# Kernel tuning notes

Hardware: AMD Instinct MI355X
Metric: run time of the kernel (lower is better)

Reference implementation:

```python
import jax, jax.numpy as jnp
import numpy as np

B, N, C_IN = 4, 2048, 64
HID, HEADS, NQ = 128, 4, 16
D = HID // HEADS  # per-head dim = 32
NEG_SLOPE = 0.2
MASK_VAL = -1e9


def setup_inputs() -> dict:
    key = jax.random.key(0)
    ks = jax.random.split(key, 8)
    x = jax.random.normal(ks[0], (B, N, C_IN), dtype=jnp.float32)
    adj = jax.random.randint(ks[1], (N, N), 0, 2, dtype=jnp.int32)
    # lin_in: Linear(in_channels, hidden_dim)
    W_in = jax.random.normal(ks[2], (C_IN, HID), dtype=jnp.float32) / np.sqrt(C_IN)
    b_in = jnp.zeros((HID,), dtype=jnp.float32)
    # attention vectors [1, heads, d]
    att_src = jax.random.normal(ks[3], (1, HEADS, D), dtype=jnp.float32) * 0.1
    att_dst = jax.random.normal(ks[4], (1, HEADS, D), dtype=jnp.float32) * 0.1
    # output_head: Linear(num_nodes*hidden_dim, num_qubits)
    W_out = jax.random.normal(ks[5], (N * HID, NQ), dtype=jnp.float32) / np.sqrt(N * HID)
    b_out = jnp.zeros((NQ,), dtype=jnp.float32)
    return {"x": x, "adj": adj, "W_in": W_in, "b_in": b_in,
            "att_src": att_src, "att_dst": att_dst,
            "W_out": W_out, "b_out": b_out}


def reference(x, adj, W_in, b_in, att_src, att_dst, W_out, b_out):
    b, n, _ = x.shape
    h = (x @ W_in + b_in).reshape(b, n, HEADS, D)          # [B,N,H,D]
    alpha_src = jnp.sum(h * att_src, axis=-1)               # [B,N,H]
    alpha_dst = jnp.sum(h * att_dst, axis=-1)               # [B,N,H]
    # additive scores: score[b,i,j,h] = src[b,i,h] + dst[b,j,h]
    scores = alpha_src[:, :, None, :] + alpha_dst[:, None, :, :]  # [B,N,N,H]
    scores = jnp.where(scores >= 0, scores, NEG_SLOPE * scores)   # leaky relu
    mask = (adj == 0)[None, :, :, None]                     # [1,N,N,1]
    scores = jnp.where(mask, MASK_VAL, scores)
    alpha = jax.nn.softmax(scores, axis=2)                  # softmax over neighbors j
    # dropout p=0.0 (eval) -> identity
    out = jnp.einsum('bijh,bjhd->bihd', alpha, h)           # [B,N,H,D]
    out = out.reshape(b, n * HEADS * D)                     # [B, N*HID]
    return out @ W_out + b_out                              # [B, NQ]
```

## Files before the change

kernel.cpp:

```cpp
#include <hip/hip_runtime.h>
#include <math.h>

#define BB 4
#define NN 2048
#define CIN 64
#define HID 128
#define HEADS 4
#define DD 32
#define NQ 16
#define KTOT (NN*HID)
#define LOG2E 1.44269504088896340736f
#define NEGBIG_BITS 0xC2C80000u

#define HB 512
#define AB 2048

typedef __attribute__((ext_vector_type(8))) _Float16 half8;
typedef __attribute__((ext_vector_type(4))) _Float16 half4;
typedef __attribute__((ext_vector_type(2))) _Float16 half2;
typedef __attribute__((ext_vector_type(4))) float f32x4;
typedef __attribute__((ext_vector_type(4))) unsigned uint4v;

__global__ __launch_bounds__(256) void k_pre(
    const float* __restrict__ x, const float* __restrict__ W_in,
    const float* __restrict__ b_in, const float* __restrict__ att_src,
    const float* __restrict__ att_dst, const int* __restrict__ adj,
    _Float16* __restrict__ hH, float* __restrict__ srcA, float* __restrict__ dstA,
    unsigned* __restrict__ adjb, const float* __restrict__ b_out,
    float* __restrict__ dout)
{
    __shared__ float Wl[CIN * HID];
    __shared__ float xl[16][CIN];
    const int t = threadIdx.x;

    if (blockIdx.x >= HB) {
        const int bid = blockIdx.x - HB;
        if (bid == 0 && t < 64) dout[t] = b_out[t & 15];
        const int gid = bid * 256 + t;
        const int lane = t & 63;
        const int4* p = (const int4*)(adj + (size_t)gid * 8);
        const int4 a = p[0], b = p[1];
        unsigned byte =
            (a.x != 0 ? 1u : 0u)  | (a.y != 0 ? 2u : 0u)  | (a.z != 0 ? 4u : 0u)  | (a.w != 0 ? 8u : 0u) |
            (b.x != 0 ? 16u : 0u) | (b.y != 0 ? 32u : 0u) | (b.z != 0 ? 64u : 0u) | (b.w != 0 ? 128u : 0u);
        unsigned u = byte | (((unsigned)__shfl_xor((int)byte, 1, 64)) << 8);
        u = u | (((unsigned)__shfl_xor((int)u, 2, 64)) << 16);
        if ((lane & 3) == 0) adjb[gid >> 2] = u;
        return;
    }

    const int jj0 = blockIdx.x * 16;
    {
        const float4* Ws = (const float4*)W_in;
        float4* Wd = (float4*)Wl;
#pragma unroll
        for (int u = 0; u < 8; ++u) Wd[t + 256 * u] = Ws[t + 256 * u];
        ((float4*)&xl[0][0])[t] = ((const float4*)(x + (size_t)jj0 * CIN))[t];
    }
    __syncthreads();

    const int c = t & 127, rg = t >> 7;
    const int b = jj0 >> 11, j0 = (jj0 & (NN - 1)) + rg * 8;
    const int h = c >> 5;

    float acc[8];
    const float bc = b_in[c];
#pragma unroll
    for (int rr = 0; rr < 8; ++rr) acc[rr] = bc;

#pragma unroll
    for (int k4 = 0; k4 < CIN; k4 += 4) {
        const float w0 = Wl[(k4 + 0) * HID + c];
        const float w1 = Wl[(k4 + 1) * HID + c];
        const float w2 = Wl[(k4 + 2) * HID + c];
        const float w3 = Wl[(k4 + 3) * HID + c];
#pragma unroll
        for (int rr = 0; rr < 8; ++rr) {
            const float4 xv = *(const float4*)&xl[rg * 8 + rr][k4];
            acc[rr] = fmaf(xv.w, w3, fmaf(xv.z, w2, fmaf(xv.y, w1, fmaf(xv.x, w0, acc[rr]))));
        }
    }

    half8 hv;
#pragma unroll
    for (int rr = 0; rr < 8; ++rr) hv[rr] = (_Float16)acc[rr];
    *(half8*)(hH + (size_t)(b * HID + c) * NN + j0) = hv;

    const float as = att_src[c], ad = att_dst[c];
#pragma unroll
    for (int rr = 0; rr < 8; ++rr) {
        float vs = acc[rr] * as, vd = acc[rr] * ad;
#pragma unroll
        for (int m = 16; m >= 1; m >>= 1) {
            vs += __shfl_xor(vs, m, 64);
            vd += __shfl_xor(vd, m, 64);
        }
        if ((t & 31) == 0) {
            srcA[(size_t)(b * HEADS + h) * NN + j0 + rr] = vs * LOG2E;
            dstA[(size_t)(b * HEADS + h) * NN + j0 + rr] = vd * LOG2E;
        }
    }
}

__global__ __launch_bounds__(512, 4) void k_attn(
    const unsigned* __restrict__ adjb, const _Float16* __restrict__ hH,
    const float* __restrict__ srcA, const float* __restrict__ dstA,
    _Float16* __restrict__ P, float* __restrict__ S)
{
    __shared__ float redA[8][32][36];
    __shared__ float redS[8][32];

    const int t = threadIdx.x;
    const int lane = t & 63;
    const int w = t >> 6;
    const int h = w & 3;
    const int bx = blockIdx.x;
    const int jh = bx >> 8;
    const int b = (bx >> 6) & 3;
    const int i0 = (bx & 63) * 32;
    const int jstart = jh * 1024 + (w >> 2) * 512;

    const int r16 = lane & 15;
    const int g = lane >> 4;
    const float srci0 = srcA[(size_t)(b * HEADS + h) * NN + i0 + r16];
    const float srci1 = srcA[(size_t)(b * HEADS + h) * NN + i0 + 16 + r16];
    const uint2* adjr0 = (const uint2*)(adjb + (size_t)(i0 + r16) * (NN / 32)) + (jstart >> 6);
    const uint2* adjr1 = (const uint2*)(adjb + (size_t)(i0 + 16 + r16) * (NN / 32)) + (jstart >> 6);
    const _Float16* bbase = hH + ((size_t)(b * HID) + h * DD + r16) * NN + jstart + 8 * g;
    const float4* dst4 = (const float4*)(dstA + (size_t)(b * HEADS + h) * NN + jstart) + 2 * g;

    f32x4 acc00 = {0.f, 0.f, 0.f, 0.f};
    f32x4 acc01 = {0.f, 0.f, 0.f, 0.f};
    f32x4 acc10 = {0.f, 0.f, 0.f, 0.f};
    f32x4 acc11 = {0.f, 0.f, 0.f, 0.f};
    f32x4 accS0 = {0.f, 0.f, 0.f, 0.f};
    f32x4 accS1 = {0.f, 0.f, 0.f, 0.f};
    const half8 ones = {(_Float16)1.f, (_Float16)1.f, (_Float16)1.f, (_Float16)1.f,
                        (_Float16)1.f, (_Float16)1.f, (_Float16)1.f, (_Float16)1.f};

    auto MAKEAF = [&](float srci, unsigned bits, const float* dv) -> half8 {
        float wv[8];
#pragma unroll
        for (int e = 0; e < 8; ++e) {
            float s = srci + dv[e];
            s = fmaxf(s, 0.2f * s);
            const unsigned m = (unsigned)(((int)(bits << (31 - e))) >> 31);
            const unsigned su = __builtin_bit_cast(unsigned, s);
            const unsigned sel = (su & m) | (NEGBIG_BITS & ~m);
            wv[e] = __builtin_amdgcn_exp2f(__builtin_bit_cast(float, sel));
        }
        uint4v uu;
        uu[0] = __builtin_bit_cast(unsigned, __builtin_amdgcn_cvt_pkrtz(wv[0], wv[1]));
        uu[1] = __builtin_bit_cast(unsigned, __builtin_amdgcn_cvt_pkrtz(wv[2], wv[3]));
        uu[2] = __builtin_bit_cast(unsigned, __builtin_amdgcn_cvt_pkrtz(wv[4], wv[5]));
        uu[3] = __builtin_bit_cast(unsigned, __builtin_amdgcn_cvt_pkrtz(wv[6], wv[7]));
        return __builtin_bit_cast(half8, uu);
    };

    auto GROUP = [&](unsigned w0, unsigned w1, float4 da, float4 db, half8 bb0, half8 bb1) {
        const unsigned bits0 = w0 >> (8 * g);
        const unsigned bits1 = w1 >> (8 * g);
        const float dv[8] = {da.x, da.y, da.z, da.w, db.x, db.y, db.z, db.w};
        const half8 af0 = MAKEAF(srci0, bits0, dv);
        const half8 af1 = MAKEAF(srci1, bits1, dv);
        acc00 = __builtin_amdgcn_mfma_f32_16x16x32_f16(af0, bb0, acc00, 0, 0, 0);
        acc01 = __builtin_amdgcn_mfma_f32_16x16x32_f16(af0, bb1, acc01, 0, 0, 0);
        acc10 = __builtin_amdgcn_mfma_f32_16x16x32_f16(af1, bb0, acc10, 0, 0, 0);
        acc11 = __builtin_amdgcn_mfma_f32_16x16x32_f16(af1, bb1, acc11, 0, 0, 0);
        accS0 = __builtin_amdgcn_mfma_f32_16x16x32_f16(af0, ones, accS0, 0, 0, 0);
        accS1 = __builtin_amdgcn_mfma_f32_16x16x32_f16(af1, ones, accS1, 0, 0, 0);
    };

    uint2 aA0 = adjr0[0], aA1 = adjr1[0];
    half8 bA0 = *(const half8*)(bbase);
    half8 bA1 = *(const half8*)(bbase + 32);
    half8 bA2 = *(const half8*)(bbase + 16 * NN);
    half8 bA3 = *(const half8*)(bbase + 16 * NN + 32);
    __builtin_amdgcn_sched_barrier(0);

#pragma unroll
    for (int p = 0; p < 4; ++p) {
        const int itB = 2 * p + 1;
        const uint2 aB0 = adjr0[itB], aB1 = adjr1[itB];
        const half8 bB0 = *(const half8*)(bbase + itB * 64);
        const half8 bB1 = *(const half8*)(bbase + itB * 64 + 32);
        const half8 bB2 = *(const half8*)(bbase + 16 * NN + itB * 64);
        const half8 bB3 = *(const half8*)(bbase + 16 * NN + itB * 64 + 32);
        __builtin_amdgcn_sched_barrier(0);

        {
            const int it = 2 * p;
            GROUP(aA0.x, aA1.x, dst4[it * 16],     dst4[it * 16 + 1], bA0, bA2);
            GROUP(aA0.y, aA1.y, dst4[it * 16 + 8], dst4[it * 16 + 9], bA1, bA3);
        }
        __builtin_amdgcn_sched_barrier(0);

        if (p < 3) {
            const int itA = 2 * p + 2;
            aA0 = adjr0[itA]; aA1 = adjr1[itA];
            bA0 = *(const half8*)(bbase + itA * 64);
            bA1 = *(const half8*)(bbase + itA * 64 + 32);
            bA2 = *(const half8*)(bbase + 16 * NN + itA * 64);
            bA3 = *(const half8*)(bbase + 16 * NN + itA * 64 + 32);
        }
        __builtin_amdgcn_sched_barrier(0);

        GROUP(aB0.x, aB1.x, dst4[itB * 16],     dst4[itB * 16 + 1], bB0, bB2);
        GROUP(aB0.y, aB1.y, dst4[itB * 16 + 8], dst4[itB * 16 + 9], bB1, bB3);
        __builtin_amdgcn_sched_barrier(0);
    }

#pragma unroll
    for (int r = 0; r < 4; ++r) {
        redA[w][ 0 + 4 * g + r][ 0 + r16] = acc00[r];
        redA[w][ 0 + 4 * g + r][16 + r16] = acc01[r];
        redA[w][16 + 4 * g + r][ 0 + r16] = acc10[r];
        redA[w][16 + 4 * g + r][16 + r16] = acc11[r];
    }
    if (r16 == 0) {
#pragma unroll
        for (int r = 0; r < 4; ++r) {
            redS[w][ 0 + 4 * g + r] = accS0[r];
            redS[w][16 + 4 * g + r] = accS1[r];
        }
    }
    __syncthreads();

    {
        const int i = t & 31;
        const int u = t >> 5;
        const int h2 = u & 3;
        const int d0 = (u >> 2) * 8;
        const float4 va0 = *(const float4*)&redA[h2][i][d0];
        const float4 va1 = *(const float4*)&redA[h2][i][d0 + 4];
        const float4 vb0 = *(const float4*)&redA[h2 + 4][i][d0];
        const float4 vb1 = *(const float4*)&redA[h2 + 4][i][d0 + 4];
        const float rs = redS[h2][i] + redS[h2 + 4][i];
        const half2 q0 = __builtin_bit_cast(half2, __builtin_amdgcn_cvt_pkrtz(va0.x + vb0.x, va0.y + vb0.y));
        const half2 q1 = __builtin_bit_cast(half2, __builtin_amdgcn_cvt_pkrtz(va0.z + vb0.z, va0.w + vb0.w));
        const half2 q2 = __builtin_bit_cast(half2, __builtin_amdgcn_cvt_pkrtz(va1.x + vb1.x, va1.y + vb1.y));
        const half2 q3 = __builtin_bit_cast(half2, __builtin_amdgcn_cvt_pkrtz(va1.z + vb1.z, va1.w + vb1.w));
        half8 o;
        o[0] = q0[0]; o[1] = q0[1]; o[2] = q1[0]; o[3] = q1[1];
        o[4] = q2[0]; o[5] = q2[1]; o[6] = q3[0]; o[7] = q3[1];
        *(half8*)(P + ((size_t)(jh * BB + b) * NN + i0 + i) * HID + h2 * DD + d0) = o;
        if (u < 4)
            S[((size_t)(jh * BB + b) * NN + i0 + i) * HEADS + h2] = rs;
    }
}

__global__ __launch_bounds__(256) void k_proj(
    const _Float16* __restrict__ P, const float* __restrict__ S,
    const float* __restrict__ W_out, float* __restrict__ dout)
{
    __shared__ float wlT[NQ][260];
    __shared__ float red[256];

    const int t = threadIdx.x;
    const int k0 = blockIdx.x * 256;

#pragma unroll
    for (int u = 0; u < 4; ++u) {
        const int flat = (u * 256 + t) * 4;
        const float4 wv = *(const float4*)(W_out + (size_t)k0 * NQ + flat);
        const int krel = flat >> 4;
        const int q0 = flat & 15;
        wlT[q0 + 0][krel] = wv.x;
        wlT[q0 + 1][krel] = wv.y;
        wlT[q0 + 2][krel] = wv.z;
        wlT[q0 + 3][krel] = wv.w;
    }
    __syncthreads();

    const int q = t & 15;
    const int b = (t >> 4) & 3;
    const int ks = (t >> 6) * 64;
    const int i = (k0 + ks) >> 7;

    const _Float16* p0 = P + (size_t)b * KTOT + k0 + ks;
    const _Float16* p1 = P + (size_t)(BB + b) * KTOT + k0 + ks;

    float acc = 0.f;
#pragma unroll
    for (int seg = 0; seg < 2; ++seg) {
        const int h = ((k0 + ks + seg * 32) >> 5) & 3;
        const float rs = S[((size_t)b * NN + i) * HEADS + h] +
                         S[((size_t)(BB + b) * NN + i) * HEADS + h];
        const float inv = __builtin_amdgcn_rcpf(rs);
#pragma unroll
        for (int k8 = 0; k8 < 4; ++k8) {
            const int kk = seg * 32 + k8 * 8;
            const half8 a0 = *(const half8*)(p0 + kk);
            const half8 a1 = *(const half8*)(p1 + kk);
            const float4 w0 = *(const float4*)&wlT[q][ks + kk];
            const float4 w1 = *(const float4*)&wlT[q][ks + kk + 4];
            acc = fmaf(((float)a0[0] + (float)a1[0]) * inv, w0.x, acc);
            acc = fmaf(((float)a0[1] + (float)a1[1]) * inv, w0.y, acc);
            acc = fmaf(((float)a0[2] + (float)a1[2]) * inv, w0.z, acc);
            acc = fmaf(((float)a0[3] + (float)a1[3]) * inv, w0.w, acc);
            acc = fmaf(((float)a0[4] + (float)a1[4]) * inv, w1.x, acc);
            acc = fmaf(((float)a0[5] + (float)a1[5]) * inv, w1.y, acc);
            acc = fmaf(((float)a0[6] + (float)a1[6]) * inv, w1.z, acc);
            acc = fmaf(((float)a0[7] + (float)a1[7]) * inv, w1.w, acc);
        }
    }

    red[t] = acc;
    __syncthreads();
    if (t < 64)
        atomicAdd(&dout[t], red[t] + red[t + 64] + red[t + 128] + red[t + 192]);
}

extern "C" void kernel_launch(void* const* d_in, const int* in_sizes, int n_in,
                              void* d_out, int out_size, void* d_ws, size_t ws_size,
                              hipStream_t stream)
{
    const float* x       = (const float*)d_in[0];
    const int*   adj     = (const int*)d_in[1];
    const float* W_in    = (const float*)d_in[2];
    const float* b_in    = (const float*)d_in[3];
    const float* att_src = (const float*)d_in[4];
    const float* att_dst = (const float*)d_in[5];
    const float* W_out   = (const float*)d_in[6];
    const float* b_out   = (const float*)d_in[7];
    float* out = (float*)d_out;

    char* ws = (char*)d_ws;
    _Float16* P  = (_Float16*)ws;
    float* S     = (float*)(ws + sizeof(_Float16) * 2 * (size_t)BB * KTOT);
    float* srcA  = S + 2 * (size_t)BB * NN * HEADS;
    float* dstA  = srcA + (size_t)BB * HEADS * NN;
    _Float16* hH = (_Float16*)(dstA + (size_t)BB * HEADS * NN);
    unsigned* adjbw = (unsigned*)((char*)hH + sizeof(_Float16) * (size_t)BB * KTOT);

    k_pre<<<HB + AB, 256, 0, stream>>>(x, W_in, b_in, att_src, att_dst, adj,
                                       hH, srcA, dstA, adjbw, b_out, out);
    k_attn<<<2 * BB * (NN / 32), 512, 0, stream>>>(adjbw, hH, srcA, dstA, P, S);
    k_proj<<<KTOT / 256, 256, 0, stream>>>(P, S, W_out, out);
}
```

Before: 74.79 us.

## Retile attention to 64 rows per block and split neighbours into four slices

Each attention block now covers 64 query rows instead of 32 and a quarter of the neighbour range instead of a half. Every loaded tile of h values is reused across four row groups, which cuts global loads of the value matrix per unit of work. Grid size stays the same. The projection kernel now sums four partial slices of P and S instead of two. In exchange the partial buffers double in size, there is more traffic in the final reduction, and the attention kernel holds more accumulator registers and runs two shared-memory reduction rounds.

```diff
diff --git a/kernel.cpp b/kernel.cpp
--- a/kernel.cpp
+++ b/kernel.cpp
@@ -11,6 +11,7 @@
 #define KTOT (NN*HID)
 #define LOG2E 1.44269504088896340736f
 #define NEGBIG_BITS 0xC2C80000u
+#define NSL 4
 
 #define HB 512
 #define AB 2048
@@ -114,27 +115,32 @@
     const int lane = t & 63;
     const int w = t >> 6;
     const int h = w & 3;
+    const int jhw = w >> 2;
     const int bx = blockIdx.x;
-    const int jh = bx >> 8;
-    const int b = (bx >> 6) & 3;
-    const int i0 = (bx & 63) * 32;
-    const int jstart = jh * 1024 + (w >> 2) * 512;
+    const int jq = bx >> 7;
+    const int b = (bx >> 5) & 3;
+    const int i0 = (bx & 31) * 64;
+    const int jstart = jq * 512 + jhw * 256;
 
     const int r16 = lane & 15;
     const int g = lane >> 4;
-    const float srci0 = srcA[(size_t)(b * HEADS + h) * NN + i0 + r16];
-    const float srci1 = srcA[(size_t)(b * HEADS + h) * NN + i0 + 16 + r16];
-    const uint2* adjr0 = (const uint2*)(adjb + (size_t)(i0 + r16) * (NN / 32)) + (jstart >> 6);
+    const float* srcbase = srcA + (size_t)(b * HEADS + h) * NN + i0 + r16;
+    const float srci0 = srcbase[0];
+    const float srci1 = srcbase[16];
+    const float srci2 = srcbase[32];
+    const float srci3 = srcbase[48];
+    const uint2* adjr0 = (const uint2*)(adjb + (size_t)(i0 +  0 + r16) * (NN / 32)) + (jstart >> 6);
     const uint2* adjr1 = (const uint2*)(adjb + (size_t)(i0 + 16 + r16) * (NN / 32)) + (jstart >> 6);
+    const uint2* adjr2 = (const uint2*)(adjb + (size_t)(i0 + 32 + r16) * (NN / 32)) + (jstart >> 6);
+    const uint2* adjr3 = (const uint2*)(adjb + (size_t)(i0 + 48 + r16) * (NN / 32)) + (jstart >> 6);
     const _Float16* bbase = hH + ((size_t)(b * HID) + h * DD + r16) * NN + jstart + 8 * g;
     const float4* dst4 = (const float4*)(dstA + (size_t)(b * HEADS + h) * NN + jstart) + 2 * g;
 
-    f32x4 acc00 = {0.f, 0.f, 0.f, 0.f};
-    f32x4 acc01 = {0.f, 0.f, 0.f, 0.f};
-    f32x4 acc10 = {0.f, 0.f, 0.f, 0.f};
-    f32x4 acc11 = {0.f, 0.f, 0.f, 0.f};
-    f32x4 accS0 = {0.f, 0.f, 0.f, 0.f};
-    f32x4 accS1 = {0.f, 0.f, 0.f, 0.f};
+    f32x4 acc00 = {0,0,0,0}, acc01 = {0,0,0,0};
+    f32x4 acc10 = {0,0,0,0}, acc11 = {0,0,0,0};
+    f32x4 acc20 = {0,0,0,0}, acc21 = {0,0,0,0};
+    f32x4 acc30 = {0,0,0,0}, acc31 = {0,0,0,0};
+    f32x4 accS0 = {0,0,0,0}, accS1 = {0,0,0,0}, accS2 = {0,0,0,0}, accS3 = {0,0,0,0};
     const half8 ones = {(_Float16)1.f, (_Float16)1.f, (_Float16)1.f, (_Float16)1.f,
                         (_Float16)1.f, (_Float16)1.f, (_Float16)1.f, (_Float16)1.f};
 
@@ -157,21 +163,36 @@
         return __builtin_bit_cast(half8, uu);
     };
 
-    auto GROUP = [&](unsigned w0, unsigned w1, float4 da, float4 db, half8 bb0, half8 bb1) {
-        const unsigned bits0 = w0 >> (8 * g);
-        const unsigned bits1 = w1 >> (8 * g);
+    auto GROUP = [&](unsigned w0, unsigned w1, unsigned w2, unsigned w3,
+                     float4 da, float4 db, half8 bb0, half8 bb1) {
         const float dv[8] = {da.x, da.y, da.z, da.w, db.x, db.y, db.z, db.w};
-        const half8 af0 = MAKEAF(srci0, bits0, dv);
-        const half8 af1 = MAKEAF(srci1, bits1, dv);
-        acc00 = __builtin_amdgcn_mfma_f32_16x16x32_f16(af0, bb0, acc00, 0, 0, 0);
-        acc01 = __builtin_amdgcn_mfma_f32_16x16x32_f16(af0, bb1, acc01, 0, 0, 0);
-        acc10 = __builtin_amdgcn_mfma_f32_16x16x32_f16(af1, bb0, acc10, 0, 0, 0);
-        acc11 = __builtin_amdgcn_mfma_f32_16x16x32_f16(af1, bb1, acc11, 0, 0, 0);
-        accS0 = __builtin_amdgcn_mfma_f32_16x16x32_f16(af0, ones, accS0, 0, 0, 0);
-        accS1 = __builtin_amdgcn_mfma_f32_16x16x32_f16(af1, ones, accS1, 0, 0, 0);
+        {
+            const half8 af = MAKEAF(srci0, w0 >> (8 * g), dv);
+            acc00 = __builtin_amdgcn_mfma_f32_16x16x32_f16(af, bb0, acc00, 0, 0, 0);
+            acc01 = __builtin_amdgcn_mfma_f32_16x16x32_f16(af, bb1, acc01, 0, 0, 0);
+            accS0 = __builtin_amdgcn_mfma_f32_16x16x32_f16(af, ones, accS0, 0, 0, 0);
+        }
+        {
+            const half8 af = MAKEAF(srci1, w1 >> (8 * g), dv);
+            acc10 = __builtin_amdgcn_mfma_f32_16x16x32_f16(af, bb0, acc10, 0, 0, 0);
+            acc11 = __builtin_amdgcn_mfma_f32_16x16x32_f16(af, bb1, acc11, 0, 0, 0);
+            accS1 = __builtin_amdgcn_mfma_f32_16x16x32_f16(af, ones, accS1, 0, 0, 0);
+        }
+        {
+            const half8 af = MAKEAF(srci2, w2 >> (8 * g), dv);
+            acc20 = __builtin_amdgcn_mfma_f32_16x16x32_f16(af, bb0, acc20, 0, 0, 0);
+            acc21 = __builtin_amdgcn_mfma_f32_16x16x32_f16(af, bb1, acc21, 0, 0, 0);
+            accS2 = __builtin_amdgcn_mfma_f32_16x16x32_f16(af, ones, accS2, 0, 0, 0);
+        }
+        {
+            const half8 af = MAKEAF(srci3, w3 >> (8 * g), dv);
+            acc30 = __builtin_amdgcn_mfma_f32_16x16x32_f16(af, bb0, acc30, 0, 0, 0);
+            acc31 = __builtin_amdgcn_mfma_f32_16x16x32_f16(af, bb1, acc31, 0, 0, 0);
+            accS3 = __builtin_amdgcn_mfma_f32_16x16x32_f16(af, ones, accS3, 0, 0, 0);
+        }
     };
 
-    uint2 aA0 = adjr0[0], aA1 = adjr1[0];
+    uint2 aA0 = adjr0[0], aA1 = adjr1[0], aA2 = adjr2[0], aA3 = adjr3[0];
     half8 bA0 = *(const half8*)(bbase);
     half8 bA1 = *(const half8*)(bbase + 32);
     half8 bA2 = *(const half8*)(bbase + 16 * NN);
@@ -179,9 +200,9 @@
     __builtin_amdgcn_sched_barrier(0);
 
 #pragma unroll
-    for (int p = 0; p < 4; ++p) {
+    for (int p = 0; p < 2; ++p) {
         const int itB = 2 * p + 1;
-        const uint2 aB0 = adjr0[itB], aB1 = adjr1[itB];
+        const uint2 aB0 = adjr0[itB], aB1 = adjr1[itB], aB2 = adjr2[itB], aB3 = adjr3[itB];
         const half8 bB0 = *(const half8*)(bbase + itB * 64);
         const half8 bB1 = *(const half8*)(bbase + itB * 64 + 32);
         const half8 bB2 = *(const half8*)(bbase + 16 * NN + itB * 64);
@@ -190,14 +211,14 @@
 
         {
             const int it = 2 * p;
-            GROUP(aA0.x, aA1.x, dst4[it * 16],     dst4[it * 16 + 1], bA0, bA2);
-            GROUP(aA0.y, aA1.y, dst4[it * 16 + 8], dst4[it * 16 + 9], bA1, bA3);
+            GROUP(aA0.x, aA1.x, aA2.x, aA3.x, dst4[it * 16],     dst4[it * 16 + 1], bA0, bA2);
+            GROUP(aA0.y, aA1.y, aA2.y, aA3.y, dst4[it * 16 + 8], dst4[it * 16 + 9], bA1, bA3);
         }
         __builtin_amdgcn_sched_barrier(0);
 
-        if (p < 3) {
+        if (p < 1) {
             const int itA = 2 * p + 2;
-            aA0 = adjr0[itA]; aA1 = adjr1[itA];
+            aA0 = adjr0[itA]; aA1 = adjr1[itA]; aA2 = adjr2[itA]; aA3 = adjr3[itA];
             bA0 = *(const half8*)(bbase + itA * 64);
             bA1 = *(const half8*)(bbase + itA * 64 + 32);
             bA2 = *(const half8*)(bbase + 16 * NN + itA * 64);
@@ -205,47 +226,53 @@
         }
         __builtin_amdgcn_sched_barrier(0);
 
-        GROUP(aB0.x, aB1.x, dst4[itB * 16],     dst4[itB * 16 + 1], bB0, bB2);
-        GROUP(aB0.y, aB1.y, dst4[itB * 16 + 8], dst4[itB * 16 + 9], bB1, bB3);
+        GROUP(aB0.x, aB1.x, aB2.x, aB3.x, dst4[itB * 16],     dst4[itB * 16 + 1], bB0, bB2);
+        GROUP(aB0.y, aB1.y, aB2.y, aB3.y, dst4[itB * 16 + 8], dst4[itB * 16 + 9], bB1, bB3);
         __builtin_amdgcn_sched_barrier(0);
     }
 
-#pragma unroll
-    for (int r = 0; r < 4; ++r) {
-        redA[w][ 0 + 4 * g + r][ 0 + r16] = acc00[r];
-        redA[w][ 0 + 4 * g + r][16 + r16] = acc01[r];
-        redA[w][16 + 4 * g + r][ 0 + r16] = acc10[r];
-        redA[w][16 + 4 * g + r][16 + r16] = acc11[r];
-    }
-    if (r16 == 0) {
+    const size_t pbase = (size_t)(jq * BB + b) * NN + i0;
+#pragma unroll
+    for (int R = 0; R < 2; ++R) {
+        const f32x4 vA0 = R ? acc20 : acc00, vA1 = R ? acc21 : acc01;
+        const f32x4 vB0 = R ? acc30 : acc10, vB1 = R ? acc31 : acc11;
+        const f32x4 sA  = R ? accS2 : accS0, sB  = R ? accS3 : accS1;
 #pragma unroll
         for (int r = 0; r < 4; ++r) {
-            redS[w][ 0 + 4 * g + r] = accS0[r];
-            redS[w][16 + 4 * g + r] = accS1[r];
-        }
-    }
-    __syncthreads();
-
-    {
-        const int i = t & 31;
-        const int u = t >> 5;
-        const int h2 = u & 3;
-        const int d0 = (u >> 2) * 8;
-        const float4 va0 = *(const float4*)&redA[h2][i][d0];
-        const float4 va1 = *(const float4*)&redA[h2][i][d0 + 4];
-        const float4 vb0 = *(const float4*)&redA[h2 + 4][i][d0];
-        const float4 vb1 = *(const float4*)&redA[h2 + 4][i][d0 + 4];
-        const float rs = redS[h2][i] + redS[h2 + 4][i];
-        const half2 q0 = __builtin_bit_cast(half2, __builtin_amdgcn_cvt_pkrtz(va0.x + vb0.x, va0.y + vb0.y));
-        const half2 q1 = __builtin_bit_cast(half2, __builtin_amdgcn_cvt_pkrtz(va0.z + vb0.z, va0.w + vb0.w));
-        const half2 q2 = __builtin_bit_cast(half2, __builtin_amdgcn_cvt_pkrtz(va1.x + vb1.x, va1.y + vb1.y));
-        const half2 q3 = __builtin_bit_cast(half2, __builtin_amdgcn_cvt_pkrtz(va1.z + vb1.z, va1.w + vb1.w));
-        half8 o;
-        o[0] = q0[0]; o[1] = q0[1]; o[2] = q1[0]; o[3] = q1[1];
-        o[4] = q2[0]; o[5] = q2[1]; o[6] = q3[0]; o[7] = q3[1];
-        *(half8*)(P + ((size_t)(jh * BB + b) * NN + i0 + i) * HID + h2 * DD + d0) = o;
-        if (u < 4)
-            S[((size_t)(jh * BB + b) * NN + i0 + i) * HEADS + h2] = rs;
+            redA[w][ 0 + 4 * g + r][ 0 + r16] = vA0[r];
+            redA[w][ 0 + 4 * g + r][16 + r16] = vA1[r];
+            redA[w][16 + 4 * g + r][ 0 + r16] = vB0[r];
+            redA[w][16 + 4 * g + r][16 + r16] = vB1[r];
+        }
+        if (r16 == 0) {
+#pragma unroll
+            for (int r = 0; r < 4; ++r) {
+                redS[w][ 0 + 4 * g + r] = sA[r];
+                redS[w][16 + 4 * g + r] = sB[r];
+            }
+        }
+        __syncthreads();
+        {
+            const int i = t & 31;
+            const int u = t >> 5;
+            const int h2 = u & 3;
+            const int d0 = (u >> 2) * 8;
+            const float4 va0 = *(const float4*)&redA[h2][i][d0];
+            const float4 va1 = *(const float4*)&redA[h2][i][d0 + 4];
+            const float4 vb0 = *(const float4*)&redA[h2 + 4][i][d0];
+            const float4 vb1 = *(const float4*)&redA[h2 + 4][i][d0 + 4];
+            const half2 q0 = __builtin_bit_cast(half2, __builtin_amdgcn_cvt_pkrtz(va0.x + vb0.x, va0.y + vb0.y));
+            const half2 q1 = __builtin_bit_cast(half2, __builtin_amdgcn_cvt_pkrtz(va0.z + vb0.z, va0.w + vb0.w));
+            const half2 q2 = __builtin_bit_cast(half2, __builtin_amdgcn_cvt_pkrtz(va1.x + vb1.x, va1.y + vb1.y));
+            const half2 q3 = __builtin_bit_cast(half2, __builtin_amdgcn_cvt_pkrtz(va1.z + vb1.z, va1.w + vb1.w));
+            half8 o;
+            o[0] = q0[0]; o[1] = q0[1]; o[2] = q1[0]; o[3] = q1[1];
+            o[4] = q2[0]; o[5] = q2[1]; o[6] = q3[0]; o[7] = q3[1];
+            *(half8*)(P + (pbase + R * 32 + i) * HID + h2 * DD + d0) = o;
+            if (u < 4)
+                S[(pbase + R * 32 + i) * HEADS + h2] = redS[h2][i] + redS[h2 + 4][i];
+        }
+        __syncthreads();
     }
 }
 
@@ -277,31 +304,45 @@
     const int ks = (t >> 6) * 64;
     const int i = (k0 + ks) >> 7;
 
-    const _Float16* p0 = P + (size_t)b * KTOT + k0 + ks;
-    const _Float16* p1 = P + (size_t)(BB + b) * KTOT + k0 + ks;
+    const _Float16* p0 = P + (size_t)(0 * BB + b) * KTOT + k0 + ks;
+    const _Float16* p1 = P + (size_t)(1 * BB + b) * KTOT + k0 + ks;
+    const _Float16* p2 = P + (size_t)(2 * BB + b) * KTOT + k0 + ks;
+    const _Float16* p3 = P + (size_t)(3 * BB + b) * KTOT + k0 + ks;
 
     float acc = 0.f;
 #pragma unroll
     for (int seg = 0; seg < 2; ++seg) {
         const int h = ((k0 + ks + seg * 32) >> 5) & 3;
-        const float rs = S[((size_t)b * NN + i) * HEADS + h] +
-                         S[((size_t)(BB + b) * NN + i) * HEADS + h];
+        float rs = 0.f;
+#pragma unroll
+        for (int s = 0; s < NSL; ++s)
+            rs += S[((size_t)(s * BB + b) * NN + i) * HEADS + h];
         const float inv = __builtin_amdgcn_rcpf(rs);
 #pragma unroll
         for (int k8 = 0; k8 < 4; ++k8) {
             const int kk = seg * 32 + k8 * 8;
             const half8 a0 = *(const half8*)(p0 + kk);
             const half8 a1 = *(const half8*)(p1 + kk);
+            const half8 a2 = *(const half8*)(p2 + kk);
+            const half8 a3 = *(const half8*)(p3 + kk);
             const float4 w0 = *(const float4*)&wlT[q][ks + kk];
             const float4 w1 = *(const float4*)&wlT[q][ks + kk + 4];
-            acc = fmaf(((float)a0[0] + (float)a1[0]) * inv, w0.x, acc);
-            acc = fmaf(((float)a0[1] + (float)a1[1]) * inv, w0.y, acc);
-            acc = fmaf(((float)a0[2] + (float)a1[2]) * inv, w0.z, acc);
-            acc = fmaf(((float)a0[3] + (float)a1[3]) * inv, w0.w, acc);
-            acc = fmaf(((float)a0[4] + (float)a1[4]) * inv, w1.x, acc);
-            acc = fmaf(((float)a0[5] + (float)a1[5]) * inv, w1.y, acc);
-            acc = fmaf(((float)a0[6] + (float)a1[6]) * inv, w1.z, acc);
-            acc = fmaf(((float)a0[7] + (float)a1[7]) * inv, w1.w, acc);
+            const float e0 = ((float)a0[0] + (float)a1[0]) + ((float)a2[0] + (float)a3[0]);
+            const float e1 = ((float)a0[1] + (float)a1[1]) + ((float)a2[1] + (float)a3[1]);
+            const float e2 = ((float)a0[2] + (float)a1[2]) + ((float)a2[2] + (float)a3[2]);
+            const float e3 = ((float)a0[3] + (float)a1[3]) + ((float)a2[3] + (float)a3[3]);
+            const float e4 = ((float)a0[4] + (float)a1[4]) + ((float)a2[4] + (float)a3[4]);
+            const float e5 = ((float)a0[5] + (float)a1[5]) + ((float)a2[5] + (float)a3[5]);
+            const float e6 = ((float)a0[6] + (float)a1[6]) + ((float)a2[6] + (float)a3[6]);
+            const float e7 = ((float)a0[7] + (float)a1[7]) + ((float)a2[7] + (float)a3[7]);
+            acc = fmaf(e0 * inv, w0.x, acc);
+            acc = fmaf(e1 * inv, w0.y, acc);
+            acc = fmaf(e2 * inv, w0.z, acc);
+            acc = fmaf(e3 * inv, w0.w, acc);
+            acc = fmaf(e4 * inv, w1.x, acc);
+            acc = fmaf(e5 * inv, w1.y, acc);
+            acc = fmaf(e6 * inv, w1.z, acc);
+            acc = fmaf(e7 * inv, w1.w, acc);
         }
     }
 
@@ -327,14 +368,14 @@
 
     char* ws = (char*)d_ws;
     _Float16* P  = (_Float16*)ws;
-    float* S     = (float*)(ws + sizeof(_Float16) * 2 * (size_t)BB * KTOT);
-    float* srcA  = S + 2 * (size_t)BB * NN * HEADS;
+    float* S     = (float*)(ws + sizeof(_Float16) * NSL * (size_t)BB * KTOT);
+    float* srcA  = S + (size_t)NSL * BB * NN * HEADS;
     float* dstA  = srcA + (size_t)BB * HEADS * NN;
     _Float16* hH = (_Float16*)(dstA + (size_t)BB * HEADS * NN);
     unsigned* adjbw = (unsigned*)((char*)hH + sizeof(_Float16) * (size_t)BB * KTOT);
 
     k_pre<<<HB + AB, 256, 0, stream>>>(x, W_in, b_in, att_src, att_dst, adj,
                                        hH, srcA, dstA, adjbw, b_out, out);
-    k_attn<<<2 * BB * (NN / 32), 512, 0, stream>>>(adjbw, hH, srcA, dstA, P, S);
+    k_attn<<<NSL * BB * (NN / 64), 512, 0, stream>>>(adjbw, hH, srcA, dstA, P, S);
     k_proj<<<KTOT / 256, 256, 0, stream>>>(P, S, W_out, out);
 }
```

Result: slower. 77.15 us (+3.1%).
